# Kernel tuning notes

Hardware: AMD Instinct MI355X
Metric: run time of the kernel (lower is better)

The kernel has to match this reference:

```python
import jax, jax.numpy as jnp
import numpy as np

N, C, T, V = 64, 64, 256, 25
R, O = C // 8, 64  # rel_channels, out_channels
ALPHA = 1.0


def setup_inputs() -> dict:
    key = jax.random.key(0)
    ks = jax.random.split(key, 10)
    s = 0.05
    return {
        "x": jax.random.normal(ks[0], (N, C, T, V), dtype=jnp.float32),
        "A": jax.random.normal(ks[1], (V, V), dtype=jnp.float32),
        "w1": jax.random.normal(ks[2], (R, C), dtype=jnp.float32) * s,
        "b1": jnp.zeros((R,), dtype=jnp.float32),
        "w2": jax.random.normal(ks[3], (R, C), dtype=jnp.float32) * s,
        "b2": jnp.zeros((R,), dtype=jnp.float32),
        "w3": jax.random.normal(ks[4], (O, C), dtype=jnp.float32) * s,
        "b3": jnp.zeros((O,), dtype=jnp.float32),
        "w4": jax.random.normal(ks[5], (O, R), dtype=jnp.float32) * s,
        "b4": jnp.zeros((O,), dtype=jnp.float32),
    }


def reference(x, A, w1, b1, w2, b2, w3, b3, w4, b4):
    # x: (N, C, T, V)
    # conv1/conv2 are 1x1 convs followed by mean over T -> (N, R, V)
    x1 = jnp.einsum('nctv,rc->nrv', x, w1) / x.shape[2] + b1[:, None]
    x2 = jnp.einsum('nctv,rc->nrv', x, w2) / x.shape[2] + b2[:, None]
    # conv3: 1x1 conv -> (N, O, T, V)
    x3 = jnp.einsum('nctv,oc->notv', x, w3) + b3[:, None, None]
    # outer-difference attention over joints: (N, R, V, V)
    att = jnp.tanh(x1[:, :, :, None] - x2[:, :, None, :])
    # conv4 channel mix (R->O), scale, add adjacency: (N, O, V, V)
    m = jnp.einsum('nruv,or->nouv', att, w4) + b4[:, None, None]
    m = m * ALPHA + A[None, None, :, :]
    # aggregation: einsum('ncuv,nctv->nctu')
    out = jnp.einsum('ncuv,nctv->nctu', m, x3)
    return out
```

## Files before the change

### kernel.cpp

```cpp
#include <hip/hip_runtime.h>

#define NN 64
#define CC 64
#define TT 256
#define VV 25
#define RR 8
#define OO 64
#define PLANE 6400

__global__ __launch_bounds__(256) void k_xsum(const float* __restrict__ x,
                                              float* __restrict__ xsum) {
  int nc = blockIdx.x;
  const float* src = x + (size_t)nc * PLANE;
  __shared__ float s[PLANE];
  int tid = threadIdx.x;
#pragma unroll
  for (int k = 0; k < 25; ++k) s[k * 256 + tid] = src[k * 256 + tid];
  __syncthreads();
  if (tid < VV) {
    float a0 = 0.f, a1 = 0.f, a2 = 0.f, a3 = 0.f;
    for (int t = 0; t < TT; t += 4) {
      a0 += s[(t + 0) * VV + tid];
      a1 += s[(t + 1) * VV + tid];
      a2 += s[(t + 2) * VV + tid];
      a3 += s[(t + 3) * VV + tid];
    }
    xsum[nc * VV + tid] = (a0 + a1) + (a2 + a3);
  }
}

__global__ void k_wt(const float* __restrict__ w3, float* __restrict__ w3t) {
  int k = blockIdx.x * 256 + threadIdx.x;
  if (k < 4096) {
    int c = k >> 6, o = k & 63;
    w3t[k] = w3[o * 64 + c];
  }
}

__global__ __launch_bounds__(256) void k_build_m(
    const float* __restrict__ xsum, const float* __restrict__ A,
    const float* __restrict__ w1, const float* __restrict__ b1,
    const float* __restrict__ w2, const float* __restrict__ b2,
    const float* __restrict__ w4, const float* __restrict__ b4,
    float* __restrict__ mp) {
  int n = blockIdx.x;
  __shared__ float xs[CC * VV];
  __shared__ float sx1[RR * VV];
  __shared__ float sx2[RR * VV];
  __shared__ float att[RR * 625];
  int tid = threadIdx.x;
  const float* xsn = xsum + n * (CC * VV);
  for (int k = tid; k < CC * VV; k += 256) xs[k] = xsn[k];
  __syncthreads();
  if (tid < RR * VV) {
    int r = tid / VV, v = tid % VV;
    float a1 = 0.f, a2 = 0.f;
#pragma unroll
    for (int c = 0; c < CC; ++c) {
      float xv = xs[c * VV + v];
      a1 = fmaf(w1[r * CC + c], xv, a1);
      a2 = fmaf(w2[r * CC + c], xv, a2);
    }
    sx1[tid] = a1 * (1.f / 256.f) + b1[r];
    sx2[tid] = a2 * (1.f / 256.f) + b2[r];
  }
  __syncthreads();
  for (int k = tid; k < RR * 625; k += 256) {
    int r = k / 625, uv = k % 625;
    int u = uv / VV, v = uv % VV;
    att[k] = tanhf(sx1[r * VV + u] - sx2[r * VV + v]);
  }
  __syncthreads();
  for (int k = tid; k < OO * 625; k += 256) {
    int o = k / 625, uv = k % 625;
    int u = uv / VV, v = uv % VV;
    float a = b4[o] + A[uv];
#pragma unroll
    for (int r = 0; r < RR; ++r) a = fmaf(w4[o * RR + r], att[r * 625 + uv], a);
    mp[(((size_t)n * OO + o) * VV + u) * 32 + v] = a;
  }
}

__global__ __launch_bounds__(256) void k_conv3(const float* __restrict__ x,
                                               const float* __restrict__ w3t,
                                               const float* __restrict__ b3,
                                               float* __restrict__ x3) {
  int n = blockIdx.y;
  int p = blockIdx.x * 256 + threadIdx.x;
  const float* xn = x + (size_t)n * CC * PLANE;
  float acc[OO];
#pragma unroll
  for (int o = 0; o < OO; ++o) acc[o] = b3[o];
#pragma unroll 2
  for (int c = 0; c < CC; ++c) {
    float xv = xn[(size_t)c * PLANE + p];
    const float* w = w3t + c * OO;
#pragma unroll
    for (int o = 0; o < OO; ++o) acc[o] = fmaf(w[o], xv, acc[o]);
  }
  float* dst = x3 + (size_t)n * OO * PLANE + p;
#pragma unroll
  for (int o = 0; o < OO; ++o) dst[(size_t)o * PLANE] = acc[o];
}

__global__ __launch_bounds__(256) void k_aggr(float* __restrict__ out,
                                              const float* __restrict__ mp) {
  int no = blockIdx.x;
  float* base = out + (size_t)no * PLANE;
  __shared__ float s[PLANE];
  int tid = threadIdx.x;
#pragma unroll
  for (int k = 0; k < 25; ++k) s[k * 256 + tid] = base[k * 256 + tid];
  __syncthreads();
  const float* m = mp + (size_t)no * (VV * 32);
  float xr[VV], orow[VV];
#pragma unroll
  for (int v = 0; v < VV; ++v) xr[v] = s[tid * VV + v];
#pragma unroll
  for (int u = 0; u < VV; ++u) {
    float a = 0.f;
#pragma unroll
    for (int v = 0; v < VV; ++v) a = fmaf(m[u * 32 + v], xr[v], a);
    orow[u] = a;
  }
#pragma unroll
  for (int u = 0; u < VV; ++u) s[tid * VV + u] = orow[u];
  __syncthreads();
#pragma unroll
  for (int k = 0; k < 25; ++k) base[k * 256 + tid] = s[k * 256 + tid];
}

extern "C" void kernel_launch(void* const* d_in, const int* in_sizes, int n_in,
                              void* d_out, int out_size, void* d_ws,
                              size_t ws_size, hipStream_t stream) {
  const float* x = (const float*)d_in[0];
  const float* A = (const float*)d_in[1];
  const float* w1 = (const float*)d_in[2];
  const float* b1 = (const float*)d_in[3];
  const float* w2 = (const float*)d_in[4];
  const float* b2 = (const float*)d_in[5];
  const float* w3 = (const float*)d_in[6];
  const float* b3 = (const float*)d_in[7];
  const float* w4 = (const float*)d_in[8];
  const float* b4 = (const float*)d_in[9];
  float* out = (float*)d_out;
  float* ws = (float*)d_ws;

  float* xsum = ws;
  float* w3t = ws + 102400;
  float* mp = ws + 106496;

  k_xsum<<<NN * CC, 256, 0, stream>>>(x, xsum);
  k_wt<<<16, 256, 0, stream>>>(w3, w3t);
  k_build_m<<<NN, 256, 0, stream>>>(xsum, A, w1, b1, w2, b2, w4, b4, mp);
  k_conv3<<<dim3(PLANE / 256, NN), 256, 0, stream>>>(x, w3t, b3, out);
  k_aggr<<<NN * OO, 256, 0, stream>>>(out, mp);
}
```

Before: 305.7 us.

## Fuse conv3 with joint aggregation and reduce xsum with wave shuffles

Merges the 1x1 conv3 and the per-(n,o) aggregation into one kernel. Each block computes 64 output channels for a tile of 32 time steps, stages them through LDS and applies the V×V mixing matrix before writing the final output. This removes the full intermediate x3 write and its re-read through global memory. The xsum kernel now reduces over T with cross-lane shuffles instead of a shared-memory copy, and the w3 transpose moves into k_build_m, saving a launch. In exchange, blocks are large (832 threads) with 64 accumulators per thread, which lowers occupancy, and only half of each wave is active during the aggregation step.

```diff
diff --git a/kernel.cpp b/kernel.cpp
--- a/kernel.cpp
+++ b/kernel.cpp
@@ -11,30 +11,25 @@
 __global__ __launch_bounds__(256) void k_xsum(const float* __restrict__ x,
                                               float* __restrict__ xsum) {
   int nc = blockIdx.x;
-  const float* src = x + (size_t)nc * PLANE;
-  __shared__ float s[PLANE];
-  int tid = threadIdx.x;
+  int t = threadIdx.x;
+  const float* row = x + (size_t)nc * PLANE + t * VV;
+  float r[VV];
 #pragma unroll
-  for (int k = 0; k < 25; ++k) s[k * 256 + tid] = src[k * 256 + tid];
+  for (int v = 0; v < VV; ++v) r[v] = row[v];
+#pragma unroll
+  for (int off = 32; off > 0; off >>= 1) {
+#pragma unroll
+    for (int v = 0; v < VV; ++v) r[v] += __shfl_xor(r[v], off, 64);
+  }
+  __shared__ float sred[4][VV];
+  int wave = t >> 6, lane = t & 63;
+  if (lane == 0) {
+#pragma unroll
+    for (int v = 0; v < VV; ++v) sred[wave][v] = r[v];
+  }
   __syncthreads();
-  if (tid < VV) {
-    float a0 = 0.f, a1 = 0.f, a2 = 0.f, a3 = 0.f;
-    for (int t = 0; t < TT; t += 4) {
-      a0 += s[(t + 0) * VV + tid];
-      a1 += s[(t + 1) * VV + tid];
-      a2 += s[(t + 2) * VV + tid];
-      a3 += s[(t + 3) * VV + tid];
-    }
-    xsum[nc * VV + tid] = (a0 + a1) + (a2 + a3);
-  }
-}
-
-__global__ void k_wt(const float* __restrict__ w3, float* __restrict__ w3t) {
-  int k = blockIdx.x * 256 + threadIdx.x;
-  if (k < 4096) {
-    int c = k >> 6, o = k & 63;
-    w3t[k] = w3[o * 64 + c];
-  }
+  if (t < VV)
+    xsum[nc * VV + t] = (sred[0][t] + sred[1][t]) + (sred[2][t] + sred[3][t]);
 }
 
 __global__ __launch_bounds__(256) void k_build_m(
@@ -42,6 +37,7 @@
     const float* __restrict__ w1, const float* __restrict__ b1,
     const float* __restrict__ w2, const float* __restrict__ b2,
     const float* __restrict__ w4, const float* __restrict__ b4,
+    const float* __restrict__ w3, float* __restrict__ w3t,
     float* __restrict__ mp) {
   int n = blockIdx.x;
   __shared__ float xs[CC * VV];
@@ -49,6 +45,10 @@
   __shared__ float sx2[RR * VV];
   __shared__ float att[RR * 625];
   int tid = threadIdx.x;
+  for (int k = tid; k < CC * OO; k += 256) {
+    int c = k >> 6, o = k & 63;
+    w3t[k] = w3[o * CC + c];
+  }
   const float* xsn = xsum + n * (CC * VV);
   for (int k = tid; k < CC * VV; k += 256) xs[k] = xsn[k];
   __syncthreads();
@@ -81,53 +81,69 @@
   }
 }
 
-__global__ __launch_bounds__(256) void k_conv3(const float* __restrict__ x,
+__global__ __launch_bounds__(832) void k_fused(const float* __restrict__ x,
                                                const float* __restrict__ w3t,
                                                const float* __restrict__ b3,
-                                               float* __restrict__ x3) {
+                                               const float* __restrict__ mp,
+                                               float* __restrict__ out) {
+  int tile = blockIdx.x;
   int n = blockIdx.y;
-  int p = blockIdx.x * 256 + threadIdx.x;
-  const float* xn = x + (size_t)n * CC * PLANE;
+  int tid = threadIdx.x;
+  int tidc = tid < 800 ? tid : 799;
+  int v = tidc % VV;
+  int t_loc = tidc / VV;
+  int wave = tid >> 6;
+  int lane = tid & 63;
+
+  __shared__ float s3[13][825];
+
+  const float* xn = x + (size_t)n * CC * PLANE + tile * 800;
   float acc[OO];
 #pragma unroll
-  for (int o = 0; o < OO; ++o) acc[o] = b3[o];
-#pragma unroll 2
+  for (int o = 0; o < OO; ++o) acc[o] = 0.f;
   for (int c = 0; c < CC; ++c) {
-    float xv = xn[(size_t)c * PLANE + p];
+    float xv = xn[(size_t)c * PLANE + tidc];
     const float* w = w3t + c * OO;
 #pragma unroll
     for (int o = 0; o < OO; ++o) acc[o] = fmaf(w[o], xv, acc[o]);
   }
-  float* dst = x3 + (size_t)n * OO * PLANE + p;
+
+  const float* mpn = mp + (size_t)n * OO * (VV * 32);
 #pragma unroll
-  for (int o = 0; o < OO; ++o) dst[(size_t)o * PLANE] = acc[o];
-}
-
-__global__ __launch_bounds__(256) void k_aggr(float* __restrict__ out,
-                                              const float* __restrict__ mp) {
-  int no = blockIdx.x;
-  float* base = out + (size_t)no * PLANE;
-  __shared__ float s[PLANE];
-  int tid = threadIdx.x;
+  for (int rnd = 0; rnd < 5; ++rnd) {
 #pragma unroll
-  for (int k = 0; k < 25; ++k) s[k * 256 + tid] = base[k * 256 + tid];
-  __syncthreads();
-  const float* m = mp + (size_t)no * (VV * 32);
-  float xr[VV], orow[VV];
+    for (int w = 0; w < 13; ++w) {
+      int o = rnd * 13 + w;
+      if (o < OO) s3[w][v * 33 + t_loc] = acc[o] + b3[o];
+    }
+    __syncthreads();
+    int o = rnd * 13 + wave;
+    bool alive = (o < OO);
+    if (alive && lane < 32) {
+      int ou = __builtin_amdgcn_readfirstlane(o);
+      const float* mrow = mpn + (size_t)ou * (VV * 32);
+      float xr[VV];
 #pragma unroll
-  for (int v = 0; v < VV; ++v) xr[v] = s[tid * VV + v];
+      for (int vv = 0; vv < VV; ++vv) xr[vv] = s3[wave][vv * 33 + lane];
 #pragma unroll
-  for (int u = 0; u < VV; ++u) {
-    float a = 0.f;
+      for (int u = 0; u < VV; ++u) {
+        float a = 0.f;
 #pragma unroll
-    for (int v = 0; v < VV; ++v) a = fmaf(m[u * 32 + v], xr[v], a);
-    orow[u] = a;
+        for (int vv = 0; vv < VV; ++vv) a = fmaf(mrow[u * 32 + vv], xr[vv], a);
+        s3[wave][lane * 25 + u] = a;
+      }
+    }
+    __syncthreads();
+    if (alive) {
+      float* outp = out + ((size_t)(n * OO + o) * TT + tile * 32) * VV;
+#pragma unroll
+      for (int k = 0; k < 13; ++k) {
+        int idx = k * 64 + lane;
+        if (idx < 800) outp[idx] = s3[wave][idx];
+      }
+    }
+    __syncthreads();
   }
-#pragma unroll
-  for (int u = 0; u < VV; ++u) s[tid * VV + u] = orow[u];
-  __syncthreads();
-#pragma unroll
-  for (int k = 0; k < 25; ++k) base[k * 256 + tid] = s[k * 256 + tid];
 }
 
 extern "C" void kernel_launch(void* const* d_in, const int* in_sizes, int n_in,
@@ -151,8 +167,7 @@
   float* mp = ws + 106496;
 
   k_xsum<<<NN * CC, 256, 0, stream>>>(x, xsum);
-  k_wt<<<16, 256, 0, stream>>>(w3, w3t);
-  k_build_m<<<NN, 256, 0, stream>>>(xsum, A, w1, b1, w2, b2, w4, b4, mp);
-  k_conv3<<<dim3(PLANE / 256, NN), 256, 0, stream>>>(x, w3t, b3, out);
-  k_aggr<<<NN * OO, 256, 0, stream>>>(out, mp);
+  k_build_m<<<NN, 256, 0, stream>>>(xsum, A, w1, b1, w2, b2, w4, b4, w3, w3t,
+                                    mp);
+  k_fused<<<dim3(8, NN), 832, 0, stream>>>(x, w3t, b3, mp, out);
 }
```

Result: slower. 376.2 us (+23.1%).
